# Performance work log

Hardware: AMD Instinct MI355X
Metric: run time of the kernel (lower is better)

Reference implementation:

```python
import jax, jax.numpy as jnp
import numpy as np

BEAMS = 2
DEPTH = 3
NEXP = 4
HID = 128
NCLS = 100
EPS = 1e-5


def _conv(x, w, b):
    y = jax.lax.conv_general_dilated(x, w, (1, 1), 'VALID',
                                     dimension_numbers=('NCHW', 'OIHW', 'NCHW'))
    return y + b.reshape(1, -1, 1, 1)


def _bn(x, g, b):
    # training-mode batch norm over (N, H, W) per channel
    m = jnp.mean(x, axis=(0, 2, 3), keepdims=True)
    v = jnp.var(x, axis=(0, 2, 3), keepdims=True)
    return (x - m) * jax.lax.rsqrt(v + EPS) * g.reshape(1, -1, 1, 1) + b.reshape(1, -1, 1, 1)


def _pool(x):
    return jax.lax.reduce_window(x, 0.0, jax.lax.add, (1, 1, 2, 2), (1, 1, 2, 2), 'VALID') * 0.25


def _backbone(x, blocks):
    h = x
    for (w, b, g, bb) in blocks:  # 3 fixed conv blocks
        h = _pool(jax.nn.relu(_bn(_conv(h, w, b), g, bb)))
    return h.reshape(h.shape[0], -1)  # [B, 128]


def _routed_mlp(h, trajectories, expert_W, expert_b):
    # h: [N, 128] with N = B*BEAMS; trajectories: [DEPTH, B, BEAMS, NEXP]
    N = h.shape[0]
    for d in range(DEPTH):
        ops = trajectories[d].reshape(N, NEXP)
        sel = jnp.argmax(ops, axis=1)                              # per-sample expert id
        all_out = jnp.einsum('nd,eod->neo', h, expert_W) + expert_b[None]  # [N, NEXP, 128]
        out = jnp.take_along_axis(all_out, sel[:, None, None], axis=1)[:, 0, :]
        mx = jnp.max(ops, axis=1, keepdims=True)
        out = out + mx - jax.lax.stop_gradient(mx)                 # straight-through router tie
        if d != DEPTH - 1:
            out = jax.nn.relu(out)
        h = out
    return h


def setup_inputs() -> dict:
    key = jax.random.key(0)
    ks = jax.random.split(key, 12)
    B = 2048
    x = jax.random.normal(ks[0], (B, 3, 32, 32), jnp.float32)
    trajectories = jax.random.uniform(ks[1], (DEPTH, B, BEAMS, NEXP), jnp.float32)
    score_values = jax.random.normal(ks[2], (B, BEAMS), jnp.float32)
    # conv blocks
    cw1 = jax.random.normal(ks[3], (32, 3, 3, 3), jnp.float32) * 0.1
    cb1 = jnp.zeros((32,), jnp.float32)
    g1 = jnp.ones((32,), jnp.float32)
    bb1 = jnp.zeros((32,), jnp.float32)
    cw2 = jax.random.normal(ks[4], (32, 32, 3, 3), jnp.float32) * 0.06
    cb2 = jnp.zeros((32,), jnp.float32)
    g2 = jnp.ones((32,), jnp.float32)
    bb2 = jnp.zeros((32,), jnp.float32)
    cw3 = jax.random.normal(ks[5], (32, 32, 3, 3), jnp.float32) * 0.06
    cb3 = jnp.zeros((32,), jnp.float32)
    g3 = jnp.ones((32,), jnp.float32)
    bb3 = jnp.zeros((32,), jnp.float32)
    # experts: 3 Linear(128,128) + Identity (eye weight, zero bias)
    eW = jax.random.normal(ks[6], (3, HID, HID), jnp.float32) * 0.05
    expert_W = jnp.concatenate([eW, jnp.eye(HID, dtype=jnp.float32)[None]], axis=0)  # [4,128,128]
    eb = jax.random.normal(ks[7], (3, HID), jnp.float32) * 0.01
    expert_b = jnp.concatenate([eb, jnp.zeros((1, HID), jnp.float32)], axis=0)       # [4,128]
    out_W = jax.random.normal(ks[8], (NCLS, HID), jnp.float32) * 0.05
    out_b = jnp.zeros((NCLS,), jnp.float32)
    return dict(x=x, trajectories=trajectories, score_values=score_values,
                cw1=cw1, cb1=cb1, g1=g1, bb1=bb1,
                cw2=cw2, cb2=cb2, g2=g2, bb2=bb2,
                cw3=cw3, cb3=cb3, g3=g3, bb3=bb3,
                expert_W=expert_W, expert_b=expert_b, out_W=out_W, out_b=out_b)


def reference(x, trajectories, score_values,
              cw1, cb1, g1, bb1, cw2, cb2, g2, bb2, cw3, cb3, g3, bb3,
              expert_W, expert_b, out_W, out_b):
    blocks = [(cw1, cb1, g1, bb1), (cw2, cb2, g2, bb2), (cw3, cb3, g3, bb3)]
    h0 = _backbone(x, blocks)                       # [B, 128]
    h = jnp.repeat(h0, BEAMS, axis=0)               # [B*BEAMS, 128], sample-major like torch expand+view
    h = _routed_mlp(h, trajectories, expert_W, expert_b)
    preds = h @ out_W.T + out_b                     # [B*BEAMS, 100]
    logp = jax.nn.log_softmax(preds, axis=1)
    return (logp, score_values)
```

## Files before the change

kernel.cpp:

```cpp
#include <hip/hip_runtime.h>
#include <math.h>

typedef unsigned short us;
typedef short s16x8 __attribute__((ext_vector_type(8)));
typedef float f32x4 __attribute__((ext_vector_type(4)));

#define EPSV 1e-5f

static __device__ inline us f2bf(float f) {
  union { float f; unsigned u; } v; v.f = f;
  unsigned r = v.u + 0x7fffu + ((v.u >> 16) & 1u);
  return (us)(r >> 16);
}

union AU { s16x8 v; us e[8]; };

__global__ __launch_bounds__(256) void prep_weights(
    const float* __restrict__ w1, const float* __restrict__ w2,
    const float* __restrict__ w3, const float* __restrict__ eW,
    const float* __restrict__ oW,
    us* __restrict__ wt1L, us* __restrict__ wt1Lb,
    us* __restrict__ wt2L, us* __restrict__ wt3L,
    us* __restrict__ ewB, us* __restrict__ owB) {
  const int gtid = blockIdx.x * 256 + threadIdx.x;
  const int G = gridDim.x * 256;
  for (int i = gtid; i < 1280; i += G) {
    const int oc = i / 40, k = i % 40, t = k >> 2, c = k & 3;
    wt1L[i] = (t < 9 && c < 3) ? f2bf(w1[oc * 27 + c * 9 + t]) : (us)0;
    wt1Lb[i] = (k < 3) ? f2bf(w1[oc * 27 + k * 9 + 8]) : (us)0;
  }
  for (int i = gtid; i < 11520; i += G) {
    const int row = i / 40, col = i % 40;
    const int tap = row >> 5, oc = row & 31;
    wt2L[i] = (col < 32) ? f2bf(w2[oc * 288 + col * 9 + tap]) : (us)0;
    wt3L[i] = (col < 32) ? f2bf(w3[oc * 288 + col * 9 + tap]) : (us)0;
  }
  for (int i = gtid; i < 49152; i += G) ewB[i] = f2bf(eW[i]);
  for (int i = gtid; i < 14336; i += G) {
    const int cls = i >> 7;
    owB[i] = (cls < 100) ? f2bf(oW[cls * 128 + (i & 127)]) : (us)0;
  }
}

__global__ __launch_bounds__(256) void finalize_stats(
    const float* __restrict__ part, const float* __restrict__ g,
    const float* __restrict__ bb, float cnt, float* __restrict__ stats) {
  __shared__ float redS[256], redQ[256];
  const int ch = blockIdx.x, tid = threadIdx.x;
  const float* ps = part + (size_t)ch * 2048;
  const float* pq = part + (size_t)(32 + ch) * 2048;
  float s = 0.f, q = 0.f;
  for (int i = tid; i < 2048; i += 256) { s += ps[i]; q += pq[i]; }
  redS[tid] = s; redQ[tid] = q;
  __syncthreads();
  for (int off = 128; off; off >>= 1) {
    if (tid < off) { redS[tid] += redS[tid + off]; redQ[tid] += redQ[tid + off]; }
    __syncthreads();
  }
  if (tid == 0) {
    const float mean = redS[0] / cnt;
    const float var = redQ[0] / cnt - mean * mean;
    const float sc = g[ch] * rsqrtf(var + EPSV);
    stats[ch] = sc;
    stats[32 + ch] = bb[ch] - mean * sc;
  }
}

static __device__ inline void stage_x_cminor(const float* xp, us* xsb4, int tid) {
#pragma unroll
  for (int k = 0; k < 4; ++k) {
    const int p = tid + k * 256;
    const float v0 = xp[p], v1 = xp[1024 + p], v2 = xp[2048 + p];
    const unsigned lo = f2bf(v0) | ((unsigned)f2bf(v1) << 16);
    const unsigned hi = (unsigned)f2bf(v2);
    *(uint2*)&xsb4[p * 4] = make_uint2(lo, hi);
  }
}

__global__ __launch_bounds__(256) void conv1_stats(
    const float* __restrict__ x, const us* __restrict__ wt1L,
    const us* __restrict__ wt1Lb, const float* __restrict__ cb,
    float* __restrict__ part1) {
  __shared__ __align__(16) us xsb4[4096];
  __shared__ float csum[32], css[32];
  const int n = blockIdx.x, tid = threadIdx.x;
  const int wave = tid >> 6, lane = tid & 63, row16 = lane & 15, kg = lane >> 4;
  stage_x_cminor(x + (size_t)n * 3072, xsb4, tid);
  if (tid < 32) { csum[tid] = 0.f; css[tid] = 0.f; }
  __syncthreads();
  const int t0 = 2 * kg, t1 = 2 * kg + 1;
  const int toff0 = ((t0 / 3) * 32 + t0 % 3) * 4;
  const int toff1 = ((t1 / 3) * 32 + t1 % 3) * 4;
  const s16x8 bf0 = *(const s16x8*)&wt1L[row16 * 40 + kg * 8];
  const s16x8 bf1 = *(const s16x8*)&wt1L[(16 + row16) * 40 + kg * 8];
  const s16x8 bb0 = *(const s16x8*)&wt1Lb[row16 * 40 + kg * 8];
  const s16x8 bb1 = *(const s16x8*)&wt1Lb[(16 + row16) * 40 + kg * 8];
  const float bias0 = cb[row16], bias1 = cb[16 + row16];
  float s0 = 0.f, ss0 = 0.f, s1 = 0.f, ss1 = 0.f;
  for (int mt = wave; mt < 57; mt += 4) {
    const int pixA = mt * 16 + row16;
    int boff = 0;
    if (pixA < 900) {
      const int w = pixA >> 2, e = pixA & 3;
      boff = ((2 * (w / 15) + (e >> 1)) * 32 + 2 * (w % 15) + (e & 1)) * 4;
    }
    AU a;
    *(uint2*)&a.e[0] = *(const uint2*)&xsb4[boff + toff0];
    *(uint2*)&a.e[4] = *(const uint2*)&xsb4[boff + toff1];
    AU a2;
#pragma unroll
    for (int j = 0; j < 8; ++j) a2.e[j] = 0;
    if (kg == 0) *(uint2*)&a2.e[0] = *(const uint2*)&xsb4[boff + 264];
    f32x4 acc0 = {bias0, bias0, bias0, bias0};
    f32x4 acc1 = {bias1, bias1, bias1, bias1};
    acc0 = __builtin_amdgcn_mfma_f32_16x16x32_bf16(a.v, bf0, acc0, 0, 0, 0);
    acc0 = __builtin_amdgcn_mfma_f32_16x16x32_bf16(a2.v, bb0, acc0, 0, 0, 0);
    acc1 = __builtin_amdgcn_mfma_f32_16x16x32_bf16(a.v, bf1, acc1, 0, 0, 0);
    acc1 = __builtin_amdgcn_mfma_f32_16x16x32_bf16(a2.v, bb1, acc1, 0, 0, 0);
#pragma unroll
    for (int r = 0; r < 4; ++r) {
      const int pix = mt * 16 + kg * 4 + r;
      if (pix < 900) {
        s0 += acc0[r]; ss0 += acc0[r] * acc0[r];
        s1 += acc1[r]; ss1 += acc1[r] * acc1[r];
      }
    }
  }
  s0 += __shfl_down(s0, 32); s0 += __shfl_down(s0, 16);
  ss0 += __shfl_down(ss0, 32); ss0 += __shfl_down(ss0, 16);
  s1 += __shfl_down(s1, 32); s1 += __shfl_down(s1, 16);
  ss1 += __shfl_down(ss1, 32); ss1 += __shfl_down(ss1, 16);
  if (lane < 16) {
    atomicAdd(&csum[row16], s0); atomicAdd(&css[row16], ss0);
    atomicAdd(&csum[16 + row16], s1); atomicAdd(&css[16 + row16], ss1);
  }
  __syncthreads();
  if (tid < 32) {
    part1[tid * 2048 + n] = csum[tid];
    part1[(32 + tid) * 2048 + n] = css[tid];
  }
}

__global__ __launch_bounds__(256) void conv1_apply_conv2_stats(
    const float* __restrict__ x, const us* __restrict__ wt1L,
    const us* __restrict__ wt1Lb, const float* __restrict__ cb1,
    const float* __restrict__ stats1,
    const us* __restrict__ wt2L, const float* __restrict__ cb2,
    float* __restrict__ part2, us* __restrict__ p1g) {
  __shared__ __align__(16) us xsb4[4096];
  __shared__ __align__(16) us p1b[9000];
  __shared__ float scS[32], shS[32], csum[32], css[32];
  const int n = blockIdx.x, tid = threadIdx.x;
  const int wave = tid >> 6, lane = tid & 63, row16 = lane & 15, kg = lane >> 4;
  stage_x_cminor(x + (size_t)n * 3072, xsb4, tid);
  if (tid < 32) {
    scS[tid] = stats1[tid]; shS[tid] = stats1[32 + tid];
    csum[tid] = 0.f; css[tid] = 0.f;
  }
  __syncthreads();
  {
    const int t0 = 2 * kg, t1 = 2 * kg + 1;
    const int toff0 = ((t0 / 3) * 32 + t0 % 3) * 4;
    const int toff1 = ((t1 / 3) * 32 + t1 % 3) * 4;
    const s16x8 bf0 = *(const s16x8*)&wt1L[row16 * 40 + kg * 8];
    const s16x8 bf1 = *(const s16x8*)&wt1L[(16 + row16) * 40 + kg * 8];
    const s16x8 bb0 = *(const s16x8*)&wt1Lb[row16 * 40 + kg * 8];
    const s16x8 bb1 = *(const s16x8*)&wt1Lb[(16 + row16) * 40 + kg * 8];
    const float bias0 = cb1[row16], bias1 = cb1[16 + row16];
    const float sc0 = scS[row16], sh0 = shS[row16];
    const float sc1 = scS[16 + row16], sh1 = shS[16 + row16];
    for (int mt = wave; mt < 57; mt += 4) {
      const int pixA = mt * 16 + row16;
      int boff = 0;
      if (pixA < 900) {
        const int w = pixA >> 2, e = pixA & 3;
        boff = ((2 * (w / 15) + (e >> 1)) * 32 + 2 * (w % 15) + (e & 1)) * 4;
      }
      AU a;
      *(uint2*)&a.e[0] = *(const uint2*)&xsb4[boff + toff0];
      *(uint2*)&a.e[4] = *(const uint2*)&xsb4[boff + toff1];
      AU a2;
#pragma unroll
      for (int j = 0; j < 8; ++j) a2.e[j] = 0;
      if (kg == 0) *(uint2*)&a2.e[0] = *(const uint2*)&xsb4[boff + 264];
      f32x4 acc0 = {bias0, bias0, bias0, bias0};
      f32x4 acc1 = {bias1, bias1, bias1, bias1};
      acc0 = __builtin_amdgcn_mfma_f32_16x16x32_bf16(a.v, bf0, acc0, 0, 0, 0);
      acc0 = __builtin_amdgcn_mfma_f32_16x16x32_bf16(a2.v, bb0, acc0, 0, 0, 0);
      acc1 = __builtin_amdgcn_mfma_f32_16x16x32_bf16(a.v, bf1, acc1, 0, 0, 0);
      acc1 = __builtin_amdgcn_mfma_f32_16x16x32_bf16(a2.v, bb1, acc1, 0, 0, 0);
      const int w = mt * 4 + kg;
      if (w < 225) {
        float p0 = 0.f, p1v = 0.f;
#pragma unroll
        for (int r = 0; r < 4; ++r) {
          p0 += fmaxf(acc0[r] * sc0 + sh0, 0.f);
          p1v += fmaxf(acc1[r] * sc1 + sh1, 0.f);
        }
        p1b[w * 40 + row16] = f2bf(p0 * 0.25f);
        p1b[w * 40 + 16 + row16] = f2bf(p1v * 0.25f);
      }
    }
  }
  __syncthreads();
  for (int i = tid; i < 900; i += 256) {
    const uint4 v = *(const uint4*)&p1b[(i >> 2) * 40 + (i & 3) * 8];
    *(uint4*)(p1g + (size_t)n * 7200 + i * 8) = v;
  }
  int inb[3];
#pragma unroll
  for (int m = 0; m < 3; ++m) {
    int pixA = (wave + 4 * m) * 16 + row16;
    if (pixA >= 169) pixA = 0;
    const int oi = pixA / 13, oj = pixA - 13 * oi;
    inb[m] = oi * 15 + oj;
  }
  const float b20 = cb2[row16], b21 = cb2[16 + row16];
  f32x4 acc[3][2];
#pragma unroll
  for (int m = 0; m < 3; ++m) {
    acc[m][0] = {b20, b20, b20, b20};
    acc[m][1] = {b21, b21, b21, b21};
  }
#pragma unroll
  for (int tap = 0; tap < 9; ++tap) {
    const int ki = tap / 3, kj = tap % 3;
    const s16x8 bf0 = *(const s16x8*)&wt2L[(tap * 32 + row16) * 40 + kg * 8];
    const s16x8 bf1 = *(const s16x8*)&wt2L[(tap * 32 + 16 + row16) * 40 + kg * 8];
#pragma unroll
    for (int m = 0; m < 3; ++m) {
      const s16x8 a = *(const s16x8*)&p1b[(inb[m] + ki * 15 + kj) * 40 + kg * 8];
      acc[m][0] = __builtin_amdgcn_mfma_f32_16x16x32_bf16(a, bf0, acc[m][0], 0, 0, 0);
      acc[m][1] = __builtin_amdgcn_mfma_f32_16x16x32_bf16(a, bf1, acc[m][1], 0, 0, 0);
    }
  }
  float s0 = 0.f, ss0 = 0.f, s1 = 0.f, ss1 = 0.f;
#pragma unroll
  for (int m = 0; m < 3; ++m)
#pragma unroll
    for (int r = 0; r < 4; ++r) {
      const int pix = (wave + 4 * m) * 16 + kg * 4 + r;
      if (pix < 169) {
        const float u0 = acc[m][0][r], u1 = acc[m][1][r];
        s0 += u0; ss0 += u0 * u0; s1 += u1; ss1 += u1 * u1;
      }
    }
  s0 += __shfl_down(s0, 32); s0 += __shfl_down(s0, 16);
  ss0 += __shfl_down(ss0, 32); ss0 += __shfl_down(ss0, 16);
  s1 += __shfl_down(s1, 32); s1 += __shfl_down(s1, 16);
  ss1 += __shfl_down(ss1, 32); ss1 += __shfl_down(ss1, 16);
  if (lane < 16) {
    atomicAdd(&csum[row16], s0); atomicAdd(&css[row16], ss0);
    atomicAdd(&csum[16 + row16], s1); atomicAdd(&css[16 + row16], ss1);
  }
  __syncthreads();
  if (tid < 32) {
    part2[tid * 2048 + n] = csum[tid];
    part2[(32 + tid) * 2048 + n] = css[tid];
  }
}

__global__ __launch_bounds__(256) void conv2_apply_conv3_stats(
    const us* __restrict__ p1g, const us* __restrict__ wt2L,
    const float* __restrict__ cb2, const float* __restrict__ stats2,
    const us* __restrict__ wt3L, const float* __restrict__ cb3,
    float* __restrict__ part3, us* __restrict__ p2g) {
  __shared__ __align__(16) us p1b[9000];
  __shared__ __align__(16) us p2b[1440];
  __shared__ float scS[32], shS[32], csum[32], css[32];
  const int n = blockIdx.x, tid = threadIdx.x;
  const int wave = tid >> 6, lane = tid & 63, row16 = lane & 15, kg = lane >> 4;
  for (int i = tid; i < 900; i += 256) {
    const uint4 v = *(const uint4*)(p1g + (size_t)n * 7200 + i * 8);
    *(uint4*)&p1b[(i >> 2) * 40 + (i & 3) * 8] = v;
  }
  if (tid < 32) {
    scS[tid] = stats2[tid]; shS[tid] = stats2[32 + tid];
    csum[tid] = 0.f; css[tid] = 0.f;
  }
  __syncthreads();
  int inb[3], mtv[3];
#pragma unroll
  for (int m = 0; m < 3; ++m) {
    const int mt = wave + 4 * m;
    mtv[m] = mt;
    const int pixA = (mt < 9) ? (mt * 16 + row16) : row16;
    const int w = pixA >> 2, e = pixA & 3;
    const int oi = 2 * (w / 6) + (e >> 1), oj = 2 * (w % 6) + (e & 1);
    inb[m] = oi * 15 + oj;
  }
  const float b20 = cb2[row16], b21 = cb2[16 + row16];
  f32x4 acc[3][2];
#pragma unroll
  for (int m = 0; m < 3; ++m) {
    acc[m][0] = {b20, b20, b20, b20};
    acc[m][1] = {b21, b21, b21, b21};
  }
#pragma unroll
  for (int tap = 0; tap < 9; ++tap) {
    const int ki = tap / 3, kj = tap % 3;
    const s16x8 bf0 = *(const s16x8*)&wt2L[(tap * 32 + row16) * 40 + kg * 8];
    const s16x8 bf1 = *(const s16x8*)&wt2L[(tap * 32 + 16 + row16) * 40 + kg * 8];
#pragma unroll
    for (int m = 0; m < 3; ++m) {
      if (mtv[m] < 9) {
        const s16x8 a = *(const s16x8*)&p1b[(inb[m] + ki * 15 + kj) * 40 + kg * 8];
        acc[m][0] = __builtin_amdgcn_mfma_f32_16x16x32_bf16(a, bf0, acc[m][0], 0, 0, 0);
        acc[m][1] = __builtin_amdgcn_mfma_f32_16x16x32_bf16(a, bf1, acc[m][1], 0, 0, 0);
      }
    }
  }
  const float sc0 = scS[row16], sh0 = shS[row16];
  const float sc1 = scS[16 + row16], sh1 = shS[16 + row16];
#pragma unroll
  for (int m = 0; m < 3; ++m) {
    if (mtv[m] < 9) {
      float p0 = 0.f, p1v = 0.f;
#pragma unroll
      for (int r = 0; r < 4; ++r) {
        p0 += fmaxf(acc[m][0][r] * sc0 + sh0, 0.f);
        p1v += fmaxf(acc[m][1][r] * sc1 + sh1, 0.f);
      }
      const int wl = mtv[m] * 4 + kg;
      p2b[wl * 40 + row16] = f2bf(p0 * 0.25f);
      p2b[wl * 40 + 16 + row16] = f2bf(p1v * 0.25f);
    }
  }
  __syncthreads();
  if (tid < 144) {
    const int row = tid >> 2, col = (tid & 3) * 8;
    const uint4 v = *(const uint4*)&p2b[row * 40 + col];
    *(uint4*)(p2g + (size_t)n * 1152 + tid * 8) = v;
  }
  __syncthreads();
  if (wave < 2) {
    const int ocb = wave * 16;
    const int inb3 = (row16 >> 2) * 6 + (row16 & 3);
    const float b3 = cb3[ocb + row16];
    f32x4 a3 = {b3, b3, b3, b3};
#pragma unroll
    for (int tap = 0; tap < 9; ++tap) {
      const int ki = tap / 3, kj = tap % 3;
      const s16x8 bf = *(const s16x8*)&wt3L[(tap * 32 + ocb + row16) * 40 + kg * 8];
      const s16x8 a = *(const s16x8*)&p2b[(inb3 + ki * 6 + kj) * 40 + kg * 8];
      a3 = __builtin_amdgcn_mfma_f32_16x16x32_bf16(a, bf, a3, 0, 0, 0);
    }
    float s = a3[0] + a3[1] + a3[2] + a3[3];
    float ss = a3[0]*a3[0] + a3[1]*a3[1] + a3[2]*a3[2] + a3[3]*a3[3];
    s += __shfl_down(s, 32); s += __shfl_down(s, 16);
    ss += __shfl_down(ss, 32); ss += __shfl_down(ss, 16);
    if (lane < 16) { atomicAdd(&csum[ocb + row16], s); atomicAdd(&css[ocb + row16], ss); }
  }
  __syncthreads();
  if (tid < 32) {
    part3[tid * 2048 + n] = csum[tid];
    part3[(32 + tid) * 2048 + n] = css[tid];
  }
}

__global__ __launch_bounds__(256) void conv3_apply(
    const us* __restrict__ p2g, const us* __restrict__ wt3L,
    const float* __restrict__ cb3, const float* __restrict__ stats3,
    float* __restrict__ h0g) {
  __shared__ __align__(16) us p2L[11520];
  __shared__ float scS[32], shS[32];
  __shared__ float h0a[1024];
  const int n0 = blockIdx.x * 8, tid = threadIdx.x;
  const int wave = tid >> 6, lane = tid & 63, row16 = lane & 15, kg = lane >> 4;
  for (int i = tid; i < 1152; i += 256) {
    const int s = i / 144, ci = i - s * 144;
    const uint4 v = *(const uint4*)(p2g + (size_t)n0 * 1152 + i * 8);
    *(uint4*)&p2L[(s * 36 + (ci >> 2)) * 40 + (ci & 3) * 8] = v;
  }
  if (tid < 32) { scS[tid] = stats3[tid]; shS[tid] = stats3[32 + tid]; }
  __syncthreads();
  const int wA = row16 >> 2, eA = row16 & 3;
  const int inb3 = (2 * (wA >> 1) + (eA >> 1)) * 6 + 2 * (wA & 1) + (eA & 1);
  const float b30 = cb3[row16], b31 = cb3[16 + row16];
  f32x4 accA[2][2];
#pragma unroll
  for (int si = 0; si < 2; ++si) {
    accA[si][0] = {b30, b30, b30, b30};
    accA[si][1] = {b31, b31, b31, b31};
  }
#pragma unroll
  for (int tap = 0; tap < 9; ++tap) {
    const int ki = tap / 3, kj = tap % 3;
    const s16x8 bf0 = *(const s16x8*)&wt3L[(tap * 32 + row16) * 40 + kg * 8];
    const s16x8 bf1 = *(const s16x8*)&wt3L[(tap * 32 + 16 + row16) * 40 + kg * 8];
#pragma unroll
    for (int si = 0; si < 2; ++si) {
      const int s = wave + 4 * si;
      const s16x8 a = *(const s16x8*)&p2L[(s * 36 + inb3 + ki * 6 + kj) * 40 + kg * 8];
      accA[si][0] = __builtin_amdgcn_mfma_f32_16x16x32_bf16(a, bf0, accA[si][0], 0, 0, 0);
      accA[si][1] = __builtin_amdgcn_mfma_f32_16x16x32_bf16(a, bf1, accA[si][1], 0, 0, 0);
    }
  }
  const float sc0 = scS[row16], sh0 = shS[row16];
  const float sc1 = scS[16 + row16], sh1 = shS[16 + row16];
#pragma unroll
  for (int si = 0; si < 2; ++si) {
    const int s = wave + 4 * si;
    float p0 = 0.f, p1v = 0.f;
#pragma unroll
    for (int r = 0; r < 4; ++r) {
      p0 += fmaxf(accA[si][0][r] * sc0 + sh0, 0.f);
      p1v += fmaxf(accA[si][1][r] * sc1 + sh1, 0.f);
    }
    h0a[s * 128 + row16 * 4 + kg] = p0 * 0.25f;
    h0a[s * 128 + (16 + row16) * 4 + kg] = p1v * 0.25f;
  }
  __syncthreads();
  ((float4*)(h0g + (size_t)n0 * 128))[tid] = ((const float4*)h0a)[tid];
}

__global__ __launch_bounds__(64) void mlp3_kernel(
    const float* __restrict__ h0, const float* __restrict__ traj,
    const us* __restrict__ ewB, const float* __restrict__ eb,
    const us* __restrict__ owB, const float* __restrict__ ob,
    float* __restrict__ out) {
  __shared__ __align__(16) us ht[16 * 136];
  __shared__ float ebl[384], obl[112];
  const int lane = threadIdx.x, row16 = lane & 15, kg = lane >> 4;
  const int rbase = blockIdx.x * 16;
  for (int i = lane; i < 384; i += 64) ebl[i] = eb[i];
  for (int i = lane; i < 112; i += 64) obl[i] = (i < 100) ? ob[i] : 0.f;
  {
    const int hr = lane >> 2, hc = (lane & 3) * 32;
    const float* hp = h0 + (size_t)((rbase + hr) >> 1) * 128 + hc;
#pragma unroll
    for (int q = 0; q < 4; ++q) {
      const float4 a0 = ((const float4*)hp)[q * 2];
      const float4 a1 = ((const float4*)hp)[q * 2 + 1];
      uint4 p;
      p.x = f2bf(a0.x) | ((unsigned)f2bf(a0.y) << 16);
      p.y = f2bf(a0.z) | ((unsigned)f2bf(a0.w) << 16);
      p.z = f2bf(a1.x) | ((unsigned)f2bf(a1.y) << 16);
      p.w = f2bf(a1.z) | ((unsigned)f2bf(a1.w) << 16);
      *(uint4*)&ht[hr * 136 + hc + q * 8] = p;
    }
  }
  __syncthreads();
  float accv[8][4];
#pragma unroll
  for (int ct = 0; ct < 8; ++ct)
#pragma unroll
    for (int r = 0; r < 4; ++r) {
      const int rowg = rbase + kg * 4 + r;
      accv[ct][r] = h0[(size_t)(rowg >> 1) * 128 + ct * 16 + row16];
    }
  for (int d = 0; d < 3; ++d) {
    int sel[4];
#pragma unroll
    for (int r = 0; r < 4; ++r) {
      const int rowg = rbase + kg * 4 + r;
      const float4 t4 = *(const float4*)(traj + d * 16384 + rowg * 4);
      int s = 0; float mx = t4.x;
      if (t4.y > mx) { mx = t4.y; s = 1; }
      if (t4.z > mx) { mx = t4.z; s = 2; }
      if (t4.w > mx) { mx = t4.w; s = 3; }
      sel[r] = s;
    }
    s16x8 a[4];
#pragma unroll
    for (int kc = 0; kc < 4; ++kc)
      a[kc] = *(const s16x8*)&ht[row16 * 136 + kc * 32 + kg * 8];
    float newacc[8][4];
#pragma unroll
    for (int ct = 0; ct < 8; ++ct)
#pragma unroll
      for (int r = 0; r < 4; ++r)
        newacc[ct][r] = (sel[r] == 3) ? accv[ct][r] : 0.f;
#pragma unroll
    for (int e = 0; e < 3; ++e) {
#pragma unroll
      for (int ct = 0; ct < 8; ++ct) {
        f32x4 t = {0.f, 0.f, 0.f, 0.f};
#pragma unroll
        for (int kc = 0; kc < 4; ++kc) {
          const s16x8 b = *(const s16x8*)&ewB[(e * 128 + ct * 16 + row16) * 128 + kc * 32 + kg * 8];
          t = __builtin_amdgcn_mfma_f32_16x16x32_bf16(a[kc], b, t, 0, 0, 0);
        }
        const float bias = ebl[e * 128 + ct * 16 + row16];
#pragma unroll
        for (int r = 0; r < 4; ++r)
          if (sel[r] == e) newacc[ct][r] = t[r] + bias;
      }
    }
#pragma unroll
    for (int ct = 0; ct < 8; ++ct)
#pragma unroll
      for (int r = 0; r < 4; ++r) {
        float v = newacc[ct][r];
        if (d < 2) v = fmaxf(v, 0.f);
        accv[ct][r] = v;
        ht[(kg * 4 + r) * 136 + ct * 16 + row16] = f2bf(v);
      }
  }
  s16x8 a[4];
#pragma unroll
  for (int kc = 0; kc < 4; ++kc)
    a[kc] = *(const s16x8*)&ht[row16 * 136 + kc * 32 + kg * 8];
  float preds[7][4];
#pragma unroll
  for (int ct = 0; ct < 7; ++ct) {
    f32x4 t = {0.f, 0.f, 0.f, 0.f};
#pragma unroll
    for (int kc = 0; kc < 4; ++kc) {
      const s16x8 b = *(const s16x8*)&owB[(ct * 16 + row16) * 128 + kc * 32 + kg * 8];
      t = __builtin_amdgcn_mfma_f32_16x16x32_bf16(a[kc], b, t, 0, 0, 0);
    }
    const float bias = obl[ct * 16 + row16];
#pragma unroll
    for (int r = 0; r < 4; ++r) preds[ct][r] = t[r] + bias;
  }
  const bool v6 = (96 + row16) < 100;
#pragma unroll
  for (int r = 0; r < 4; ++r) {
    float mx = -INFINITY;
#pragma unroll
    for (int ct = 0; ct < 7; ++ct)
      if (ct < 6 || v6) mx = fmaxf(mx, preds[ct][r]);
    mx = fmaxf(mx, __shfl_xor(mx, 1)); mx = fmaxf(mx, __shfl_xor(mx, 2));
    mx = fmaxf(mx, __shfl_xor(mx, 4)); mx = fmaxf(mx, __shfl_xor(mx, 8));
    float s = 0.f;
#pragma unroll
    for (int ct = 0; ct < 7; ++ct)
      if (ct < 6 || v6) s += expf(preds[ct][r] - mx);
    s += __shfl_xor(s, 1); s += __shfl_xor(s, 2);
    s += __shfl_xor(s, 4); s += __shfl_xor(s, 8);
    const float lg = mx + logf(s);
    const int rowg = rbase + kg * 4 + r;
#pragma unroll
    for (int ct = 0; ct < 7; ++ct)
      if (ct < 6 || v6) out[(size_t)rowg * 100 + ct * 16 + row16] = preds[ct][r] - lg;
  }
}

extern "C" void kernel_launch(void* const* d_in, const int* in_sizes, int n_in,
                              void* d_out, int out_size, void* d_ws, size_t ws_size,
                              hipStream_t stream) {
  const float* x     = (const float*)d_in[0];
  const float* traj  = (const float*)d_in[1];
  const float* score = (const float*)d_in[2];
  const float* cw1 = (const float*)d_in[3];
  const float* cb1 = (const float*)d_in[4];
  const float* g1  = (const float*)d_in[5];
  const float* bb1 = (const float*)d_in[6];
  const float* cw2 = (const float*)d_in[7];
  const float* cb2 = (const float*)d_in[8];
  const float* g2  = (const float*)d_in[9];
  const float* bb2 = (const float*)d_in[10];
  const float* cw3 = (const float*)d_in[11];
  const float* cb3 = (const float*)d_in[12];
  const float* g3  = (const float*)d_in[13];
  const float* bb3 = (const float*)d_in[14];
  const float* eW  = (const float*)d_in[15];
  const float* eb  = (const float*)d_in[16];
  const float* oW  = (const float*)d_in[17];
  const float* ob  = (const float*)d_in[18];
  float* out = (float*)d_out;

  char* ws = (char*)d_ws;
  float* stats1 = (float*)ws;
  float* stats2 = (float*)(ws + 256);
  float* stats3 = (float*)(ws + 512);
  us* wt1L  = (us*)(ws + 1024);
  us* wt1Lb = (us*)(ws + 4096);
  us* wt2L  = (us*)(ws + 8192);
  us* wt3L  = (us*)(ws + 8192 + 23040);
  us* ewB   = (us*)(ws + 65536);
  us* owB   = (us*)(ws + 65536 + 98304);
  us* p1g   = (us*)(ws + 262144);
  us* p2g   = (us*)(ws + 262144 + 29491200);
  float* h0g = (float*)(ws + 262144 + 29491200 + 4718592);
  char* pbase = ws + 262144 + 29491200 + 4718592 + 1048576;
  float* part1 = (float*)pbase;
  float* part2 = (float*)(pbase + 524288);
  float* part3 = (float*)(pbase + 1048576);

  prep_weights<<<64, 256, 0, stream>>>(cw1, cw2, cw3, eW, oW,
                                       wt1L, wt1Lb, wt2L, wt3L, ewB, owB);
  conv1_stats<<<2048, 256, 0, stream>>>(x, wt1L, wt1Lb, cb1, part1);
  finalize_stats<<<32, 256, 0, stream>>>(part1, g1, bb1, 2048.f * 900.f, stats1);
  conv1_apply_conv2_stats<<<2048, 256, 0, stream>>>(x, wt1L, wt1Lb, cb1, stats1,
                                                    wt2L, cb2, part2, p1g);
  finalize_stats<<<32, 256, 0, stream>>>(part2, g2, bb2, 2048.f * 169.f, stats2);
  conv2_apply_conv3_stats<<<2048, 256, 0, stream>>>(p1g, wt2L, cb2, stats2,
                                                    wt3L, cb3, part3, p2g);
  finalize_stats<<<32, 256, 0, stream>>>(part3, g3, bb3, 2048.f * 16.f, stats3);
  conv3_apply<<<256, 256, 0, stream>>>(p2g, wt3L, cb3, stats3, h0g);
  mlp3_kernel<<<256, 64, 0, stream>>>(h0g, traj, ewB, eb, owB, ob, out);
  hipMemcpyAsync(out + 409600, score, 4096 * sizeof(float),
                 hipMemcpyDeviceToDevice, stream);
}
```

Baseline: 119.3 us.

## Store raw conv2 outputs instead of pooled conv1, fuse conv3 apply into MLP

The conv1-apply kernel now writes conv2 pre-BN outputs in bf16, grouped by pool window, instead of writing the pooled conv1 map. That removes the second conv2 recompute, which previously re-read 7200 elements per sample. A new kernel applies BN2, ReLU and pooling, runs conv3 stats over 8 samples per block, and needs only a 256-partial finalize. The conv3 apply step is fused with the routed MLP, so the h0 global round-trip and one launch go away. The trade-off is bf16 rounding of the conv2 outputs before BN and a single-wave conv3 apply that runs 8 samples serially.

```diff
diff --git a/kernel.cpp b/kernel.cpp
--- a/kernel.cpp
+++ b/kernel.cpp
@@ -12,6 +12,8 @@
   unsigned r = v.u + 0x7fffu + ((v.u >> 16) & 1u);
   return (us)(r >> 16);
 }
+static __device__ inline float bflo(unsigned u) { return __uint_as_float(u << 16); }
+static __device__ inline float bfhi(unsigned u) { return __uint_as_float(u & 0xffff0000u); }
 
 union AU { s16x8 v; us e[8]; };
 
@@ -146,7 +148,7 @@
     const us* __restrict__ wt1Lb, const float* __restrict__ cb1,
     const float* __restrict__ stats1,
     const us* __restrict__ wt2L, const float* __restrict__ cb2,
-    float* __restrict__ part2, us* __restrict__ p1g) {
+    float* __restrict__ part2, us* __restrict__ y2s) {
   __shared__ __align__(16) us xsb4[4096];
   __shared__ __align__(16) us p1b[9000];
   __shared__ float scS[32], shS[32], csum[32], css[32];
@@ -203,16 +205,20 @@
     }
   }
   __syncthreads();
-  for (int i = tid; i < 900; i += 256) {
-    const uint4 v = *(const uint4*)&p1b[(i >> 2) * 40 + (i & 3) * 8];
-    *(uint4*)(p1g + (size_t)n * 7200 + i * 8) = v;
-  }
-  int inb[3];
+  int inb[3], mtv[3];
 #pragma unroll
   for (int m = 0; m < 3; ++m) {
-    int pixA = (wave + 4 * m) * 16 + row16;
-    if (pixA >= 169) pixA = 0;
-    const int oi = pixA / 13, oj = pixA - 13 * oi;
+    const int mt = wave + 4 * m;
+    mtv[m] = mt;
+    const int q = mt * 16 + row16;
+    int oi = 0, oj = 0;
+    if (q < 144) {
+      const int w = q >> 2, e = q & 3;
+      oi = 2 * (w / 6) + (e >> 1); oj = 2 * (w % 6) + (e & 1);
+    } else if (q < 169) {
+      const int r = q - 144;
+      if (r < 13) { oi = 12; oj = r; } else { oi = r - 13; oj = 12; }
+    }
     inb[m] = oi * 15 + oj;
   }
   const float b20 = cb2[row16], b21 = cb2[16 + row16];
@@ -229,22 +235,37 @@
     const s16x8 bf1 = *(const s16x8*)&wt2L[(tap * 32 + 16 + row16) * 40 + kg * 8];
 #pragma unroll
     for (int m = 0; m < 3; ++m) {
-      const s16x8 a = *(const s16x8*)&p1b[(inb[m] + ki * 15 + kj) * 40 + kg * 8];
-      acc[m][0] = __builtin_amdgcn_mfma_f32_16x16x32_bf16(a, bf0, acc[m][0], 0, 0, 0);
-      acc[m][1] = __builtin_amdgcn_mfma_f32_16x16x32_bf16(a, bf1, acc[m][1], 0, 0, 0);
+      if (mtv[m] < 11) {
+        const s16x8 a = *(const s16x8*)&p1b[(inb[m] + ki * 15 + kj) * 40 + kg * 8];
+        acc[m][0] = __builtin_amdgcn_mfma_f32_16x16x32_bf16(a, bf0, acc[m][0], 0, 0, 0);
+        acc[m][1] = __builtin_amdgcn_mfma_f32_16x16x32_bf16(a, bf1, acc[m][1], 0, 0, 0);
+      }
     }
   }
   float s0 = 0.f, ss0 = 0.f, s1 = 0.f, ss1 = 0.f;
 #pragma unroll
-  for (int m = 0; m < 3; ++m)
-#pragma unroll
-    for (int r = 0; r < 4; ++r) {
-      const int pix = (wave + 4 * m) * 16 + kg * 4 + r;
-      if (pix < 169) {
-        const float u0 = acc[m][0][r], u1 = acc[m][1][r];
-        s0 += u0; ss0 += u0 * u0; s1 += u1; ss1 += u1 * u1;
-      }
-    }
+  for (int m = 0; m < 3; ++m) {
+    if (mtv[m] < 11) {
+      if (mtv[m] < 9) {
+        const int w = mtv[m] * 4 + kg;
+        uint2 pk0, pk1;
+        pk0.x = f2bf(acc[m][0][0]) | ((unsigned)f2bf(acc[m][0][1]) << 16);
+        pk0.y = f2bf(acc[m][0][2]) | ((unsigned)f2bf(acc[m][0][3]) << 16);
+        pk1.x = f2bf(acc[m][1][0]) | ((unsigned)f2bf(acc[m][1][1]) << 16);
+        pk1.y = f2bf(acc[m][1][2]) | ((unsigned)f2bf(acc[m][1][3]) << 16);
+        *(uint2*)(y2s + (((size_t)n * 36 + w) * 32 + row16) * 4) = pk0;
+        *(uint2*)(y2s + (((size_t)n * 36 + w) * 32 + 16 + row16) * 4) = pk1;
+      }
+#pragma unroll
+      for (int r = 0; r < 4; ++r) {
+        const int q = mtv[m] * 16 + kg * 4 + r;
+        if (q < 169) {
+          const float u0 = acc[m][0][r], u1 = acc[m][1][r];
+          s0 += u0; ss0 += u0 * u0; s1 += u1; ss1 += u1 * u1;
+        }
+      }
+    }
+  }
   s0 += __shfl_down(s0, 32); s0 += __shfl_down(s0, 16);
   ss0 += __shfl_down(ss0, 32); ss0 += __shfl_down(ss0, 16);
   s1 += __shfl_down(s1, 32); s1 += __shfl_down(s1, 16);
@@ -260,195 +281,165 @@
   }
 }
 
-__global__ __launch_bounds__(256) void conv2_apply_conv3_stats(
-    const us* __restrict__ p1g, const us* __restrict__ wt2L,
-    const float* __restrict__ cb2, const float* __restrict__ stats2,
+__global__ __launch_bounds__(256) void bnpool2_conv3_stats(
+    const us* __restrict__ y2s, const float* __restrict__ stats2,
     const us* __restrict__ wt3L, const float* __restrict__ cb3,
     float* __restrict__ part3, us* __restrict__ p2g) {
-  __shared__ __align__(16) us p1b[9000];
-  __shared__ __align__(16) us p2b[1440];
+  __shared__ __align__(16) us p2L[11520];
   __shared__ float scS[32], shS[32], csum[32], css[32];
-  const int n = blockIdx.x, tid = threadIdx.x;
+  const int n0 = blockIdx.x * 8, tid = threadIdx.x;
   const int wave = tid >> 6, lane = tid & 63, row16 = lane & 15, kg = lane >> 4;
-  for (int i = tid; i < 900; i += 256) {
-    const uint4 v = *(const uint4*)(p1g + (size_t)n * 7200 + i * 8);
-    *(uint4*)&p1b[(i >> 2) * 40 + (i & 3) * 8] = v;
-  }
   if (tid < 32) {
     scS[tid] = stats2[tid]; shS[tid] = stats2[32 + tid];
     csum[tid] = 0.f; css[tid] = 0.f;
   }
   __syncthreads();
-  int inb[3], mtv[3];
-#pragma unroll
-  for (int m = 0; m < 3; ++m) {
-    const int mt = wave + 4 * m;
-    mtv[m] = mt;
-    const int pixA = (mt < 9) ? (mt * 16 + row16) : row16;
-    const int w = pixA >> 2, e = pixA & 3;
-    const int oi = 2 * (w / 6) + (e >> 1), oj = 2 * (w % 6) + (e & 1);
-    inb[m] = oi * 15 + oj;
-  }
-  const float b20 = cb2[row16], b21 = cb2[16 + row16];
-  f32x4 acc[3][2];
-#pragma unroll
-  for (int m = 0; m < 3; ++m) {
-    acc[m][0] = {b20, b20, b20, b20};
-    acc[m][1] = {b21, b21, b21, b21};
-  }
-#pragma unroll
-  for (int tap = 0; tap < 9; ++tap) {
-    const int ki = tap / 3, kj = tap % 3;
-    const s16x8 bf0 = *(const s16x8*)&wt2L[(tap * 32 + row16) * 40 + kg * 8];
-    const s16x8 bf1 = *(const s16x8*)&wt2L[(tap * 32 + 16 + row16) * 40 + kg * 8];
-#pragma unroll
-    for (int m = 0; m < 3; ++m) {
-      if (mtv[m] < 9) {
-        const s16x8 a = *(const s16x8*)&p1b[(inb[m] + ki * 15 + kj) * 40 + kg * 8];
-        acc[m][0] = __builtin_amdgcn_mfma_f32_16x16x32_bf16(a, bf0, acc[m][0], 0, 0, 0);
-        acc[m][1] = __builtin_amdgcn_mfma_f32_16x16x32_bf16(a, bf1, acc[m][1], 0, 0, 0);
-      }
-    }
-  }
-  const float sc0 = scS[row16], sh0 = shS[row16];
-  const float sc1 = scS[16 + row16], sh1 = shS[16 + row16];
-#pragma unroll
-  for (int m = 0; m < 3; ++m) {
-    if (mtv[m] < 9) {
-      float p0 = 0.f, p1v = 0.f;
-#pragma unroll
-      for (int r = 0; r < 4; ++r) {
-        p0 += fmaxf(acc[m][0][r] * sc0 + sh0, 0.f);
-        p1v += fmaxf(acc[m][1][r] * sc1 + sh1, 0.f);
-      }
-      const int wl = mtv[m] * 4 + kg;
-      p2b[wl * 40 + row16] = f2bf(p0 * 0.25f);
-      p2b[wl * 40 + 16 + row16] = f2bf(p1v * 0.25f);
-    }
-  }
-  __syncthreads();
-  if (tid < 144) {
-    const int row = tid >> 2, col = (tid & 3) * 8;
-    const uint4 v = *(const uint4*)&p2b[row * 40 + col];
-    *(uint4*)(p2g + (size_t)n * 1152 + tid * 8) = v;
-  }
-  __syncthreads();
-  if (wave < 2) {
-    const int ocb = wave * 16;
-    const int inb3 = (row16 >> 2) * 6 + (row16 & 3);
-    const float b3 = cb3[ocb + row16];
-    f32x4 a3 = {b3, b3, b3, b3};
+#pragma unroll
+  for (int it = 0; it < 36; ++it) {
+    const int i = tid + it * 256;
+    const int c = i & 31, w = (i >> 5) % 36, s = i / 1152;
+    const uint2 v = *(const uint2*)(y2s + (((size_t)(n0 + s) * 36 + w) * 32 + c) * 4);
+    const float sc = scS[c], sh = shS[c];
+    const float p = fmaxf(bflo(v.x) * sc + sh, 0.f) + fmaxf(bfhi(v.x) * sc + sh, 0.f) +
+                    fmaxf(bflo(v.y) * sc + sh, 0.f) + fmaxf(bfhi(v.y) * sc + sh, 0.f);
+    const us pb = f2bf(p * 0.25f);
+    p2L[(s * 36 + w) * 40 + c] = pb;
+    p2g[((size_t)(n0 + s) * 36 + w) * 32 + c] = pb;
+  }
+  __syncthreads();
+  const int inb3 = (row16 >> 2) * 6 + (row16 & 3);
+  const float b30 = cb3[row16], b31 = cb3[16 + row16];
+  float s0 = 0.f, ss0 = 0.f, s1 = 0.f, ss1 = 0.f;
+#pragma unroll
+  for (int si = 0; si < 2; ++si) {
+    const int s = wave * 2 + si;
+    f32x4 a0 = {b30, b30, b30, b30};
+    f32x4 a1 = {b31, b31, b31, b31};
 #pragma unroll
     for (int tap = 0; tap < 9; ++tap) {
       const int ki = tap / 3, kj = tap % 3;
-      const s16x8 bf = *(const s16x8*)&wt3L[(tap * 32 + ocb + row16) * 40 + kg * 8];
-      const s16x8 a = *(const s16x8*)&p2b[(inb3 + ki * 6 + kj) * 40 + kg * 8];
-      a3 = __builtin_amdgcn_mfma_f32_16x16x32_bf16(a, bf, a3, 0, 0, 0);
-    }
-    float s = a3[0] + a3[1] + a3[2] + a3[3];
-    float ss = a3[0]*a3[0] + a3[1]*a3[1] + a3[2]*a3[2] + a3[3]*a3[3];
-    s += __shfl_down(s, 32); s += __shfl_down(s, 16);
-    ss += __shfl_down(ss, 32); ss += __shfl_down(ss, 16);
-    if (lane < 16) { atomicAdd(&csum[ocb + row16], s); atomicAdd(&css[ocb + row16], ss); }
+      const s16x8 bf0 = *(const s16x8*)&wt3L[(tap * 32 + row16) * 40 + kg * 8];
+      const s16x8 bf1 = *(const s16x8*)&wt3L[(tap * 32 + 16 + row16) * 40 + kg * 8];
+      const s16x8 a = *(const s16x8*)&p2L[(s * 36 + inb3 + ki * 6 + kj) * 40 + kg * 8];
+      a0 = __builtin_amdgcn_mfma_f32_16x16x32_bf16(a, bf0, a0, 0, 0, 0);
+      a1 = __builtin_amdgcn_mfma_f32_16x16x32_bf16(a, bf1, a1, 0, 0, 0);
+    }
+#pragma unroll
+    for (int r = 0; r < 4; ++r) {
+      s0 += a0[r]; ss0 += a0[r] * a0[r];
+      s1 += a1[r]; ss1 += a1[r] * a1[r];
+    }
+  }
+  s0 += __shfl_down(s0, 32); s0 += __shfl_down(s0, 16);
+  ss0 += __shfl_down(ss0, 32); ss0 += __shfl_down(ss0, 16);
+  s1 += __shfl_down(s1, 32); s1 += __shfl_down(s1, 16);
+  ss1 += __shfl_down(ss1, 32); ss1 += __shfl_down(ss1, 16);
+  if (lane < 16) {
+    atomicAdd(&csum[row16], s0); atomicAdd(&css[row16], ss0);
+    atomicAdd(&csum[16 + row16], s1); atomicAdd(&css[16 + row16], ss1);
   }
   __syncthreads();
   if (tid < 32) {
-    part3[tid * 2048 + n] = csum[tid];
-    part3[(32 + tid) * 2048 + n] = css[tid];
-  }
-}
-
-__global__ __launch_bounds__(256) void conv3_apply(
+    part3[tid * 2048 + n0 / 8] = csum[tid];
+    part3[(32 + tid) * 2048 + n0 / 8] = css[tid];
+  }
+}
+
+__global__ __launch_bounds__(256) void finalize_stats256(
+    const float* __restrict__ part, const float* __restrict__ g,
+    const float* __restrict__ bb, float cnt, float* __restrict__ stats) {
+  __shared__ float redS[256], redQ[256];
+  const int ch = blockIdx.x, tid = threadIdx.x;
+  const float* ps = part + (size_t)ch * 2048;
+  const float* pq = part + (size_t)(32 + ch) * 2048;
+  float s = 0.f, q = 0.f;
+  if (tid < 256) {  }
+  s = (tid < 256) ? ps[tid] : 0.f;
+  q = (tid < 256) ? pq[tid] : 0.f;
+  redS[tid] = s; redQ[tid] = q;
+  __syncthreads();
+  for (int off = 128; off; off >>= 1) {
+    if (tid < off) { redS[tid] += redS[tid + off]; redQ[tid] += redQ[tid + off]; }
+    __syncthreads();
+  }
+  if (tid == 0) {
+    const float mean = redS[0] / cnt;
+    const float var = redQ[0] / cnt - mean * mean;
+    const float sc = g[ch] * rsqrtf(var + EPSV);
+    stats[ch] = sc;
+    stats[32 + ch] = bb[ch] - mean * sc;
+  }
+}
+
+__global__ __launch_bounds__(64) void conv3_apply_mlp(
     const us* __restrict__ p2g, const us* __restrict__ wt3L,
     const float* __restrict__ cb3, const float* __restrict__ stats3,
-    float* __restrict__ h0g) {
+    const float* __restrict__ traj,
+    const us* __restrict__ ewB, const float* __restrict__ eb,
+    const us* __restrict__ owB, const float* __restrict__ ob,
+    float* __restrict__ out) {
   __shared__ __align__(16) us p2L[11520];
-  __shared__ float scS[32], shS[32];
   __shared__ float h0a[1024];
-  const int n0 = blockIdx.x * 8, tid = threadIdx.x;
-  const int wave = tid >> 6, lane = tid & 63, row16 = lane & 15, kg = lane >> 4;
-  for (int i = tid; i < 1152; i += 256) {
+  __shared__ __align__(16) us ht[16 * 136];
+  __shared__ float scS[32], shS[32], ebl[384], obl[112];
+  const int lane = threadIdx.x, row16 = lane & 15, kg = lane >> 4;
+  const int n0 = blockIdx.x * 8, rbase = blockIdx.x * 16;
+  for (int i = lane; i < 1152; i += 64) {
     const int s = i / 144, ci = i - s * 144;
-    const uint4 v = *(const uint4*)(p2g + (size_t)n0 * 1152 + i * 8);
+    const uint4 v = ((const uint4*)(p2g + (size_t)n0 * 1152))[i];
     *(uint4*)&p2L[(s * 36 + (ci >> 2)) * 40 + (ci & 3) * 8] = v;
   }
-  if (tid < 32) { scS[tid] = stats3[tid]; shS[tid] = stats3[32 + tid]; }
+  if (lane < 32) { scS[lane] = stats3[lane]; shS[lane] = stats3[32 + lane]; }
+  for (int i = lane; i < 384; i += 64) ebl[i] = eb[i];
+  for (int i = lane; i < 112; i += 64) obl[i] = (i < 100) ? ob[i] : 0.f;
   __syncthreads();
   const int wA = row16 >> 2, eA = row16 & 3;
   const int inb3 = (2 * (wA >> 1) + (eA >> 1)) * 6 + 2 * (wA & 1) + (eA & 1);
   const float b30 = cb3[row16], b31 = cb3[16 + row16];
-  f32x4 accA[2][2];
-#pragma unroll
-  for (int si = 0; si < 2; ++si) {
-    accA[si][0] = {b30, b30, b30, b30};
-    accA[si][1] = {b31, b31, b31, b31};
-  }
-#pragma unroll
-  for (int tap = 0; tap < 9; ++tap) {
-    const int ki = tap / 3, kj = tap % 3;
-    const s16x8 bf0 = *(const s16x8*)&wt3L[(tap * 32 + row16) * 40 + kg * 8];
-    const s16x8 bf1 = *(const s16x8*)&wt3L[(tap * 32 + 16 + row16) * 40 + kg * 8];
-#pragma unroll
-    for (int si = 0; si < 2; ++si) {
-      const int s = wave + 4 * si;
-      const s16x8 a = *(const s16x8*)&p2L[(s * 36 + inb3 + ki * 6 + kj) * 40 + kg * 8];
-      accA[si][0] = __builtin_amdgcn_mfma_f32_16x16x32_bf16(a, bf0, accA[si][0], 0, 0, 0);
-      accA[si][1] = __builtin_amdgcn_mfma_f32_16x16x32_bf16(a, bf1, accA[si][1], 0, 0, 0);
-    }
-  }
   const float sc0 = scS[row16], sh0 = shS[row16];
   const float sc1 = scS[16 + row16], sh1 = shS[16 + row16];
 #pragma unroll
-  for (int si = 0; si < 2; ++si) {
-    const int s = wave + 4 * si;
+  for (int s = 0; s < 8; ++s) {
+    f32x4 a0 = {b30, b30, b30, b30};
+    f32x4 a1 = {b31, b31, b31, b31};
+#pragma unroll
+    for (int tap = 0; tap < 9; ++tap) {
+      const int ki = tap / 3, kj = tap % 3;
+      const s16x8 bf0 = *(const s16x8*)&wt3L[(tap * 32 + row16) * 40 + kg * 8];
+      const s16x8 bf1 = *(const s16x8*)&wt3L[(tap * 32 + 16 + row16) * 40 + kg * 8];
+      const s16x8 a = *(const s16x8*)&p2L[(s * 36 + inb3 + ki * 6 + kj) * 40 + kg * 8];
+      a0 = __builtin_amdgcn_mfma_f32_16x16x32_bf16(a, bf0, a0, 0, 0, 0);
+      a1 = __builtin_amdgcn_mfma_f32_16x16x32_bf16(a, bf1, a1, 0, 0, 0);
+    }
     float p0 = 0.f, p1v = 0.f;
 #pragma unroll
     for (int r = 0; r < 4; ++r) {
-      p0 += fmaxf(accA[si][0][r] * sc0 + sh0, 0.f);
-      p1v += fmaxf(accA[si][1][r] * sc1 + sh1, 0.f);
+      p0 += fmaxf(a0[r] * sc0 + sh0, 0.f);
+      p1v += fmaxf(a1[r] * sc1 + sh1, 0.f);
     }
     h0a[s * 128 + row16 * 4 + kg] = p0 * 0.25f;
     h0a[s * 128 + (16 + row16) * 4 + kg] = p1v * 0.25f;
   }
   __syncthreads();
-  ((float4*)(h0g + (size_t)n0 * 128))[tid] = ((const float4*)h0a)[tid];
-}
-
-__global__ __launch_bounds__(64) void mlp3_kernel(
-    const float* __restrict__ h0, const float* __restrict__ traj,
-    const us* __restrict__ ewB, const float* __restrict__ eb,
-    const us* __restrict__ owB, const float* __restrict__ ob,
-    float* __restrict__ out) {
-  __shared__ __align__(16) us ht[16 * 136];
-  __shared__ float ebl[384], obl[112];
-  const int lane = threadIdx.x, row16 = lane & 15, kg = lane >> 4;
-  const int rbase = blockIdx.x * 16;
-  for (int i = lane; i < 384; i += 64) ebl[i] = eb[i];
-  for (int i = lane; i < 112; i += 64) obl[i] = (i < 100) ? ob[i] : 0.f;
-  {
-    const int hr = lane >> 2, hc = (lane & 3) * 32;
-    const float* hp = h0 + (size_t)((rbase + hr) >> 1) * 128 + hc;
-#pragma unroll
-    for (int q = 0; q < 4; ++q) {
-      const float4 a0 = ((const float4*)hp)[q * 2];
-      const float4 a1 = ((const float4*)hp)[q * 2 + 1];
-      uint4 p;
-      p.x = f2bf(a0.x) | ((unsigned)f2bf(a0.y) << 16);
-      p.y = f2bf(a0.z) | ((unsigned)f2bf(a0.w) << 16);
-      p.z = f2bf(a1.x) | ((unsigned)f2bf(a1.y) << 16);
-      p.w = f2bf(a1.z) | ((unsigned)f2bf(a1.w) << 16);
-      *(uint4*)&ht[hr * 136 + hc + q * 8] = p;
-    }
-  }
-  __syncthreads();
+#pragma unroll
+  for (int q = 0; q < 4; ++q) {
+    const int u = lane + q * 64;
+    const int lr = u >> 4, d8 = (u & 15) * 8;
+    const float* hp = &h0a[(lr >> 1) * 128 + d8];
+    uint4 p;
+    p.x = f2bf(hp[0]) | ((unsigned)f2bf(hp[1]) << 16);
+    p.y = f2bf(hp[2]) | ((unsigned)f2bf(hp[3]) << 16);
+    p.z = f2bf(hp[4]) | ((unsigned)f2bf(hp[5]) << 16);
+    p.w = f2bf(hp[6]) | ((unsigned)f2bf(hp[7]) << 16);
+    *(uint4*)&ht[lr * 136 + d8] = p;
+  }
   float accv[8][4];
 #pragma unroll
   for (int ct = 0; ct < 8; ++ct)
 #pragma unroll
-    for (int r = 0; r < 4; ++r) {
-      const int rowg = rbase + kg * 4 + r;
-      accv[ct][r] = h0[(size_t)(rowg >> 1) * 128 + ct * 16 + row16];
-    }
+    for (int r = 0; r < 4; ++r)
+      accv[ct][r] = h0a[((kg * 4 + r) >> 1) * 128 + ct * 16 + row16];
+  __syncthreads();
   for (int d = 0; d < 3; ++d) {
     int sel[4];
 #pragma unroll
@@ -571,10 +562,9 @@
   us* wt3L  = (us*)(ws + 8192 + 23040);
   us* ewB   = (us*)(ws + 65536);
   us* owB   = (us*)(ws + 65536 + 98304);
-  us* p1g   = (us*)(ws + 262144);
-  us* p2g   = (us*)(ws + 262144 + 29491200);
-  float* h0g = (float*)(ws + 262144 + 29491200 + 4718592);
-  char* pbase = ws + 262144 + 29491200 + 4718592 + 1048576;
+  us* y2s   = (us*)(ws + 262144);
+  us* p2g   = (us*)(ws + 262144 + 18874368);
+  char* pbase = ws + 262144 + 18874368 + 4718592;
   float* part1 = (float*)pbase;
   float* part2 = (float*)(pbase + 524288);
   float* part3 = (float*)(pbase + 1048576);
@@ -584,13 +574,12 @@
   conv1_stats<<<2048, 256, 0, stream>>>(x, wt1L, wt1Lb, cb1, part1);
   finalize_stats<<<32, 256, 0, stream>>>(part1, g1, bb1, 2048.f * 900.f, stats1);
   conv1_apply_conv2_stats<<<2048, 256, 0, stream>>>(x, wt1L, wt1Lb, cb1, stats1,
-                                                    wt2L, cb2, part2, p1g);
+                                                    wt2L, cb2, part2, y2s);
   finalize_stats<<<32, 256, 0, stream>>>(part2, g2, bb2, 2048.f * 169.f, stats2);
-  conv2_apply_conv3_stats<<<2048, 256, 0, stream>>>(p1g, wt2L, cb2, stats2,
-                                                    wt3L, cb3, part3, p2g);
-  finalize_stats<<<32, 256, 0, stream>>>(part3, g3, bb3, 2048.f * 16.f, stats3);
-  conv3_apply<<<256, 256, 0, stream>>>(p2g, wt3L, cb3, stats3, h0g);
-  mlp3_kernel<<<256, 64, 0, stream>>>(h0g, traj, ewB, eb, owB, ob, out);
+  bnpool2_conv3_stats<<<256, 256, 0, stream>>>(y2s, stats2, wt3L, cb3, part3, p2g);
+  finalize_stats256<<<32, 256, 0, stream>>>(part3, g3, bb3, 2048.f * 16.f, stats3);
+  conv3_apply_mlp<<<256, 64, 0, stream>>>(p2g, wt3L, cb3, stats3, traj,
+                                          ewB, eb, owB, ob, out);
   hipMemcpyAsync(out + 409600, score, 4096 * sizeof(float),
                  hipMemcpyDeviceToDevice, stream);
 }
```

After: 120.7 us. Within noise of the previous version (+1.2%).
